# Kernel optimization log

Hardware: AMD Instinct MI355X
Metric: run time of the kernel (lower is better)

Reference implementation:

```python
import jax, jax.numpy as jnp
import numpy as np

NEG_INF = -jnp.inf


def setup_inputs() -> dict:
    key = jax.random.key(0)
    k1, k2, k3 = jax.random.split(key, 3)
    b, d, n_classes = 8192, 512, 100
    x = jax.random.normal(k1, (b, d), dtype=jnp.float32)
    y = jax.random.randint(k2, (b,), 0, n_classes, dtype=jnp.int64)
    T = jax.random.uniform(k3, (), dtype=jnp.float32)
    return {"x": x, "y": y, "T": T}


def reference(x, y, T):
    b = x.shape[0]
    # normalize by (unbiased, like torch) std of the whole tensor
    xs = x / jnp.std(x, ddof=1)
    # pairwise euclidean distance via gram matrix: ||xi-xj||^2 = ni + nj - 2 xi.xj
    sqn = jnp.sum(xs * xs, axis=1)                      # [b]
    sqd = sqn[:, None] + sqn[None, :] - 2.0 * (xs @ xs.T)  # [b, b]
    sqd = jnp.maximum(sqd, 0.0)
    eye = jnp.eye(b, dtype=bool)
    # diagonal is masked out later; replace 0 with 1 before sqrt for safe grads
    dist = jnp.sqrt(jnp.where(eye, 1.0, sqd))           # [b, b]
    e_dist = -dist * jnp.power(10.0, T)                 # [b, b]
    # denominator: all pairs except self
    den_dist = jnp.where(eye, NEG_INF, e_dist)
    # numerator: same-label pairs except self (inv=False)
    same = (y[:, None] == y[None, :]) & (~eye)
    num_dist = jnp.where(same, e_dist, NEG_INF)
    num = jax.nn.logsumexp(num_dist, axis=1)            # [b]
    den = jax.nn.logsumexp(den_dist, axis=1)            # [b]
    # rows with no positives (num = -inf) are zeroed out, as in the torch code
    bad = jnp.isinf(num)
    num = jnp.where(bad, 0.0, num)
    den = jnp.where(bad, 0.0, den)
    return -jnp.mean(num - den)
```

## Files before the change

### kernel.cpp

```cpp
#include <hip/hip_runtime.h>


#define NROW 8192
#define NDIM 512
#define BM   128
#define BK   32
#define NKT  (NDIM / BK)
#define NT   (NROW / BM)
#define NBLK (NT * (NT + 1) / 2)
#define TILE (BM * BK)

typedef __attribute__((ext_vector_type(8))) short bf16x8;
typedef __attribute__((ext_vector_type(4))) float f32x4;

#define NEG_INF (-__builtin_inff())

static const size_t WS_SCAL = 4096;
static const size_t WS_XB   = 8192;
static const size_t WS_SQN  = WS_XB + (size_t)NROW * NDIM * 2;
static const size_t WS_RS   = WS_SQN + (size_t)NROW * 4;
static const size_t WS_P4   = WS_RS + (size_t)NROW * 4;

__device__ __forceinline__ unsigned short f2bf(float f) {
    unsigned int u = __float_as_uint(f);
    u += 0x7FFFu + ((u >> 16) & 1u);
    return (unsigned short)(u >> 16);
}

#define GLD_LDS16(gp, lp) __builtin_amdgcn_global_load_lds( \
    (const __attribute__((address_space(1))) unsigned int*)(gp), \
    (__attribute__((address_space(3))) unsigned int*)(lp), 16, 0, 0)

__global__ __launch_bounds__(256) void k_norm(const float* __restrict__ x,
                                              unsigned short* __restrict__ xb,
                                              float* __restrict__ sqn,
                                              float* __restrict__ rsum) {
    int w = threadIdx.x >> 6, lane = threadIdx.x & 63;
    int row = blockIdx.x * 4 + w;
    const float4* xr = (const float4*)(x + (size_t)row * NDIM);
    ushort4* xo = (ushort4*)(xb + (size_t)row * NDIM);
    float ss = 0.f, s1 = 0.f;
#pragma unroll
    for (int ph = 0; ph < 2; ++ph) {
        float4 v = xr[ph * 64 + lane];
        ss += v.x * v.x + v.y * v.y + v.z * v.z + v.w * v.w;
        s1 += (v.x + v.y) + (v.z + v.w);
        xo[ph * 64 + lane] = make_ushort4(f2bf(v.x), f2bf(v.y), f2bf(v.z), f2bf(v.w));
    }
#pragma unroll
    for (int off = 32; off >= 1; off >>= 1) {
        ss += __shfl_xor(ss, off, 64);
        s1 += __shfl_xor(s1, off, 64);
    }
    if (lane == 0) { sqn[row] = ss; rsum[row] = s1; }
}

__global__ __launch_bounds__(256) void k_prep(const float* __restrict__ sqn,
                                              const float* __restrict__ rsum,
                                              float* __restrict__ scal,
                                              float* __restrict__ out) {
    int t = threadIdx.x;
    double s = 0.0, ss = 0.0;
    for (int i = t; i < NROW; i += 256) { s += (double)rsum[i]; ss += (double)sqn[i]; }
#pragma unroll
    for (int off = 32; off >= 1; off >>= 1) {
        s  += __shfl_xor(s, off, 64);
        ss += __shfl_xor(ss, off, 64);
    }
    __shared__ double sa[4], sb[4];
    int w = t >> 6, lane = t & 63;
    if (lane == 0) { sa[w] = s; sb[w] = ss; }
    __syncthreads();
    if (t == 0) {
        double S = sa[0] + sa[1] + sa[2] + sa[3];
        double SS = sb[0] + sb[1] + sb[2] + sb[3];
        const double N = (double)NROW * (double)NDIM;
        double var = (SS - S * S / N) / (N - 1.0);
        scal[0] = (float)(1.0 / sqrt(var));
        out[0] = 0.f;
    }
}

__global__ __launch_bounds__(256, 3) void k_main(const unsigned short* __restrict__ xb,
                                                 const float* __restrict__ sqn,
                                                 const int* __restrict__ y,
                                                 const float* __restrict__ Tp,
                                                 const float* __restrict__ scal,
                                                 float4* __restrict__ part) {
    __shared__ __attribute__((aligned(16))) unsigned short lds[3][2][TILE];
    float4* P    = (float4*)&lds[0][0][0];
    float4* redC = P + 2048;

    int bid = blockIdx.x;
    int L = (bid & 7) * (NBLK / 8) + (bid >> 3);
    int RT = 0;
    for (;;) { int cnt = 36 + 64 * (7 - RT); if (L < cnt) break; L -= cnt; ++RT; }
    int rt, ct;
    if (L < 36) {
        int i = 0;
        while (L >= 8 - i) { L -= 8 - i; ++i; }
        rt = RT * 8 + i; ct = RT * 8 + i + L;
    } else {
        L -= 36;
        int CT = RT + 1 + (L >> 6), cc = L & 63;
        rt = RT * 8 + (cc >> 3); ct = CT * 8 + (cc & 7);
    }
    const bool diag = (rt == ct);

    const int tid = threadIdx.x;
    const int w = tid >> 6, lane = tid & 63;
    const int wr = w >> 1, wc = w & 1;
    const int g = lane >> 4, qq = lane & 15;
    const int rowTile = rt * BM, colTile = ct * BM;

    const int q0 = w * 2, q1 = w * 2 + 1;
    const int colg = ((lane & 3) ^ ((lane >> 3) & 3)) * 8;
    const int sr = lane >> 2;
    const unsigned short* gA0 = xb + (size_t)(rowTile + q0 * 16 + sr) * NDIM + colg;
    const unsigned short* gA1 = xb + (size_t)(rowTile + q1 * 16 + sr) * NDIM + colg;
    const unsigned short* gB0 = xb + (size_t)(colTile + q0 * 16 + sr) * NDIM + colg;
    const unsigned short* gB1 = xb + (size_t)(colTile + q1 * 16 + sr) * NDIM + colg;

#define STAGE_T(buf, ke) do { \
    GLD_LDS16(gA0 + (ke), &lds[buf][0][q0 * 512]); \
    GLD_LDS16(gA1 + (ke), &lds[buf][0][q1 * 512]); \
    GLD_LDS16(gB0 + (ke), &lds[buf][1][q0 * 512]); \
    GLD_LDS16(gB1 + (ke), &lds[buf][1][q1 * 512]); } while (0)

    const int kx = (g ^ ((qq >> 1) & 3)) * 8;
    const int aoff = (wr * 64 + qq) * BK + kx;
    const int boff = (wc * 64 + qq) * BK + kx;

    f32x4 acc[4][4];
    const f32x4 zero = {0.f, 0.f, 0.f, 0.f};
#pragma unroll
    for (int i = 0; i < 4; ++i)
#pragma unroll
        for (int j = 0; j < 4; ++j) acc[i][j] = zero;

    STAGE_T(0, 0);
    STAGE_T(1, BK);

    int c = 0;
    for (int kt = 0; kt < NKT; ++kt) {
        if (kt + 2 < NKT) {
            int sb = c + 2; if (sb >= 3) sb -= 3;
            STAGE_T(sb, (kt + 2) * BK);
            asm volatile("s_waitcnt vmcnt(8)" ::: "memory");
        } else if (kt + 1 < NKT) {
            asm volatile("s_waitcnt vmcnt(4)" ::: "memory");
        } else {
            asm volatile("s_waitcnt vmcnt(0)" ::: "memory");
        }
        __builtin_amdgcn_s_barrier();

        const unsigned short* AA = &lds[c][0][0];
        const unsigned short* BB = &lds[c][1][0];
        bf16x8 af[4], bfr[4];
#pragma unroll
        for (int mi = 0; mi < 4; ++mi)
            af[mi] = *(const bf16x8*)&AA[aoff + mi * 16 * BK];
#pragma unroll
        for (int ni = 0; ni < 4; ++ni)
            bfr[ni] = *(const bf16x8*)&BB[boff + ni * 16 * BK];
        __builtin_amdgcn_s_setprio(1);
#pragma unroll
        for (int mi = 0; mi < 4; ++mi)
#pragma unroll
            for (int ni = 0; ni < 4; ++ni)
                acc[mi][ni] = __builtin_amdgcn_mfma_f32_16x16x32_bf16(
                    af[mi], bfr[ni], acc[mi][ni], 0, 0, 0);
        __builtin_amdgcn_s_setprio(0);
        asm volatile("s_waitcnt lgkmcnt(0)" ::: "memory");
        __builtin_amdgcn_s_barrier();
        c += 1; if (c == 3) c = 0;
    }

    const float c2 = scal[0] * __builtin_amdgcn_exp2f(Tp[0] * 3.321928094887362f)
                             * 1.4426950408889634f;
    float scol[4]; int ycol[4];
#pragma unroll
    for (int ni = 0; ni < 4; ++ni) {
        int C = colTile + wc * 64 + ni * 16 + qq;
        scol[ni] = sqn[C];
        ycol[ni] = y[C];
    }

    unsigned mm0 = 0, mm1 = 0;
#pragma unroll
    for (int mi = 0; mi < 4; ++mi) {
        float srow4[4]; int yrow4[4];
#pragma unroll
        for (int r = 0; r < 4; ++r) {
            int R = rowTile + wr * 64 + mi * 16 + g * 4 + r;
            srow4[r] = sqn[R];
            yrow4[r] = y[R];
        }
#pragma unroll
        for (int r = 0; r < 4; ++r) {
            const int R = rowTile + wr * 64 + mi * 16 + g * 4 + r;
#pragma unroll
            for (int ni = 0; ni < 4; ++ni) {
                const int C = colTile + wc * 64 + ni * 16 + qq;
                float sq = fmaf(-2.f, acc[mi][ni][r], srow4[r] + scol[ni]);
                sq = fmaxf(sq, 0.f);
                float s2 = -__builtin_amdgcn_sqrtf(sq) * c2;
                if (R == C) s2 = NEG_INF;
                acc[mi][ni][r] = s2;
                unsigned bit = (yrow4[r] == ycol[ni]) ? 1u : 0u;
                int idx = ((mi & 1) * 4 + r) * 4 + ni;
                if (mi < 2) mm0 |= bit << idx; else mm1 |= bit << idx;
            }
        }
    }

    if (wr == 0) {
#pragma unroll
        for (int mi = 0; mi < 4; ++mi) {
            unsigned mmw = (mi < 2) ? mm0 : mm1;
#pragma unroll
            for (int r = 0; r < 4; ++r) {
                float m_l = fmaxf(fmaxf(acc[mi][0][r], acc[mi][1][r]),
                                  fmaxf(acc[mi][2][r], acc[mi][3][r]));
                float ld = 0.f, ln = 0.f;
#pragma unroll
                for (int ni = 0; ni < 4; ++ni) {
                    float e = __builtin_amdgcn_exp2f(acc[mi][ni][r] - m_l);
                    ld += e;
                    ln += ((mmw >> (((mi & 1) * 4 + r) * 4 + ni)) & 1) ? e : 0.f;
                }
                int lr = mi * 16 + g * 4 + r;
                P[(wc * 16 + qq) * 64 + (lr ^ qq)] = make_float4(m_l, ld, ln, 0.f);
            }
        }
    }
    __syncthreads();
    if (w == 0) {
        float M = NEG_INF, Ls = 0.f, Ln = 0.f;
#pragma unroll
        for (int wcx = 0; wcx < 2; ++wcx)
#pragma unroll
            for (int q = 0; q < 16; ++q) {
                float4 p = P[(wcx * 16 + q) * 64 + (lane ^ q)];
                if (p.x > M) {
                    float s = __builtin_amdgcn_exp2f(M - p.x);
                    Ls *= s; Ln *= s; M = p.x;
                }
                float e = __builtin_amdgcn_exp2f(p.x - M);
                Ls += p.y * e; Ln += p.z * e;
            }
        part[(size_t)ct * NROW + rowTile + lane] = make_float4(M, Ls, Ln, 0.f);
    }
    __syncthreads();
    if (wr == 1) {
#pragma unroll
        for (int mi = 0; mi < 4; ++mi) {
            unsigned mmw = (mi < 2) ? mm0 : mm1;
#pragma unroll
            for (int r = 0; r < 4; ++r) {
                float m_l = fmaxf(fmaxf(acc[mi][0][r], acc[mi][1][r]),
                                  fmaxf(acc[mi][2][r], acc[mi][3][r]));
                float ld = 0.f, ln = 0.f;
#pragma unroll
                for (int ni = 0; ni < 4; ++ni) {
                    float e = __builtin_amdgcn_exp2f(acc[mi][ni][r] - m_l);
                    ld += e;
                    ln += ((mmw >> (((mi & 1) * 4 + r) * 4 + ni)) & 1) ? e : 0.f;
                }
                int lr = mi * 16 + g * 4 + r;
                P[(wc * 16 + qq) * 64 + (lr ^ qq)] = make_float4(m_l, ld, ln, 0.f);
            }
        }
    }
    __syncthreads();
    if (w == 2) {
        float M = NEG_INF, Ls = 0.f, Ln = 0.f;
#pragma unroll
        for (int wcx = 0; wcx < 2; ++wcx)
#pragma unroll
            for (int q = 0; q < 16; ++q) {
                float4 p = P[(wcx * 16 + q) * 64 + (lane ^ q)];
                if (p.x > M) {
                    float s = __builtin_amdgcn_exp2f(M - p.x);
                    Ls *= s; Ln *= s; M = p.x;
                }
                float e = __builtin_amdgcn_exp2f(p.x - M);
                Ls += p.y * e; Ln += p.z * e;
            }
        part[(size_t)ct * NROW + rowTile + 64 + lane] = make_float4(M, Ls, Ln, 0.f);
    }

    if (!diag) {
        __syncthreads();
#pragma unroll
        for (int ni = 0; ni < 4; ++ni) {
            float mx = NEG_INF;
#pragma unroll
            for (int mi = 0; mi < 4; ++mi)
#pragma unroll
                for (int r = 0; r < 4; ++r) mx = fmaxf(mx, acc[mi][ni][r]);
            mx = fmaxf(mx, __shfl_xor(mx, 16, 64));
            mx = fmaxf(mx, __shfl_xor(mx, 32, 64));
            float ld = 0.f, ln = 0.f;
#pragma unroll
            for (int mi = 0; mi < 4; ++mi) {
                unsigned mmw = (mi < 2) ? mm0 : mm1;
#pragma unroll
                for (int r = 0; r < 4; ++r) {
                    float e = __builtin_amdgcn_exp2f(acc[mi][ni][r] - mx);
                    ld += e;
                    ln += ((mmw >> (((mi & 1) * 4 + r) * 4 + ni)) & 1) ? e : 0.f;
                }
            }
            ld += __shfl_xor(ld, 16, 64); ld += __shfl_xor(ld, 32, 64);
            ln += __shfl_xor(ln, 16, 64); ln += __shfl_xor(ln, 32, 64);
            if (g == 0) {
                int lc = wc * 64 + ni * 16 + qq;
                redC[lc * 2 + wr] = make_float4(mx, ld, ln, 0.f);
            }
        }
        __syncthreads();
        if (tid < BM) {
            float4 a = redC[tid * 2 + 0], b = redC[tid * 2 + 1];
            float M = fmaxf(a.x, b.x);
            float e0 = __builtin_amdgcn_exp2f(a.x - M), e1 = __builtin_amdgcn_exp2f(b.x - M);
            part[(size_t)rt * NROW + colTile + tid] =
                make_float4(M, a.y * e0 + b.y * e1, a.z * e0 + b.z * e1, 0.f);
        }
    }
#undef STAGE_T
}

__global__ __launch_bounds__(256) void k_rows(const float4* __restrict__ part,
                                              float* __restrict__ out) {
    int r = blockIdx.x * 256 + threadIdx.x;
    float M = NEG_INF, Ls = 0.f, Ln = 0.f;
    for (int ctt = 0; ctt < NT; ++ctt) {
        float4 p = part[(size_t)ctt * NROW + r];
        if (p.x > M) {
            float sc = __builtin_amdgcn_exp2f(M - p.x);
            Ls *= sc; Ln *= sc; M = p.x;
        }
        float s2 = __builtin_amdgcn_exp2f(p.x - M);
        Ls += p.y * s2;
        Ln += p.z * s2;
    }
    float v = (Ln > 0.f) ? (__builtin_amdgcn_logf(Ln) - __builtin_amdgcn_logf(Ls))
                               * 0.69314718055994530942f
                         : 0.f;
#pragma unroll
    for (int off = 32; off >= 1; off >>= 1) v += __shfl_xor(v, off, 64);
    __shared__ float sa[4];
    int w = threadIdx.x >> 6, lane = threadIdx.x & 63;
    if (lane == 0) sa[w] = v;
    __syncthreads();
    if (threadIdx.x == 0)
        atomicAdd(out, -((sa[0] + sa[1] + sa[2] + sa[3]) / (float)NROW));
}

extern "C" void kernel_launch(void* const* d_in, const int* in_sizes, int n_in,
                              void* d_out, int out_size, void* d_ws, size_t ws_size,
                              hipStream_t stream) {
    (void)in_sizes; (void)n_in; (void)out_size; (void)ws_size;
    const float* x  = (const float*)d_in[0];
    const int*   y  = (const int*)d_in[1];
    const float* Tp = (const float*)d_in[2];
    float* out = (float*)d_out;

    char* ws = (char*)d_ws;
    float*          scal = (float*)(ws + WS_SCAL);
    unsigned short* xb   = (unsigned short*)(ws + WS_XB);
    float*          sqn  = (float*)(ws + WS_SQN);
    float*          rsum = (float*)(ws + WS_RS);
    float4*         p4   = (float4*)(ws + WS_P4);

    k_norm <<<NROW / 4, 256, 0, stream>>>(x, xb, sqn, rsum);
    k_prep <<<1, 256, 0, stream>>>(sqn, rsum, scal, out);
    k_main <<<NBLK, 256, 0, stream>>>(xb, sqn, y, Tp, scal, p4);
    k_rows <<<NROW / 256, 256, 0, stream>>>(p4, out);
}
```

Before: 99.96 us.

## Use a single tile-wide max for logsumexp partials and share exps

Rather than computing separate per-row and per-column maxima and exponentials, the epilogue now reduces one maximum over the whole 128x128 tile and exponentiates each score once. Those exponentials feed both the row and column partial sums. This removes the duplicated exp pass for the transposed (column) contribution, drops several barriers by merging the two half-tile reduction phases, and shrinks the LDS records to float2. The trade-off is numerical: entries far below the tile maximum can underflow to zero where a per-row maximum would have kept them, and a row whose only positives are tiny could then lose them.

Result: faster. 82.93 us, median of 2 (-17.0%).

```diff
diff --git a/kernel.cpp b/kernel.cpp
--- a/kernel.cpp
+++ b/kernel.cpp
@@ -88,8 +88,9 @@
                                                  const float* __restrict__ scal,
                                                  float4* __restrict__ part) {
     __shared__ __attribute__((aligned(16))) unsigned short lds[3][2][TILE];
-    float4* P    = (float4*)&lds[0][0][0];
-    float4* redC = P + 2048;
+    float2* P    = (float2*)&lds[0][0][0];
+    float2* redC = (float2*)((char*)&lds[0][0][0] + 32768);
+    float*  mxw  = (float*)((char*)&lds[0][0][0] + 34816);
 
     int bid = blockIdx.x;
     int L = (bid & 7) * (NBLK / 8) + (bid >> 3);
@@ -187,6 +188,7 @@
     }
 
     unsigned mm0 = 0, mm1 = 0;
+    float tmax = NEG_INF;
 #pragma unroll
     for (int mi = 0; mi < 4; ++mi) {
         float srow4[4]; int yrow4[4];
@@ -207,126 +209,74 @@
                 float s2 = -__builtin_amdgcn_sqrtf(sq) * c2;
                 if (R == C) s2 = NEG_INF;
                 acc[mi][ni][r] = s2;
+                tmax = fmaxf(tmax, s2);
                 unsigned bit = (yrow4[r] == ycol[ni]) ? 1u : 0u;
                 int idx = ((mi & 1) * 4 + r) * 4 + ni;
                 if (mi < 2) mm0 |= bit << idx; else mm1 |= bit << idx;
             }
         }
     }
-
-    if (wr == 0) {
-#pragma unroll
-        for (int mi = 0; mi < 4; ++mi) {
-            unsigned mmw = (mi < 2) ? mm0 : mm1;
-#pragma unroll
-            for (int r = 0; r < 4; ++r) {
-                float m_l = fmaxf(fmaxf(acc[mi][0][r], acc[mi][1][r]),
-                                  fmaxf(acc[mi][2][r], acc[mi][3][r]));
-                float ld = 0.f, ln = 0.f;
-#pragma unroll
-                for (int ni = 0; ni < 4; ++ni) {
-                    float e = __builtin_amdgcn_exp2f(acc[mi][ni][r] - m_l);
-                    ld += e;
-                    ln += ((mmw >> (((mi & 1) * 4 + r) * 4 + ni)) & 1) ? e : 0.f;
-                }
-                int lr = mi * 16 + g * 4 + r;
-                P[(wc * 16 + qq) * 64 + (lr ^ qq)] = make_float4(m_l, ld, ln, 0.f);
+#pragma unroll
+    for (int off = 1; off <= 32; off <<= 1) tmax = fmaxf(tmax, __shfl_xor(tmax, off, 64));
+    if (lane == 0) mxw[w] = tmax;
+    __syncthreads();
+    const float Mt = fmaxf(fmaxf(mxw[0], mxw[1]), fmaxf(mxw[2], mxw[3]));
+
+#pragma unroll
+    for (int mi = 0; mi < 4; ++mi) {
+        unsigned mmw = (mi < 2) ? mm0 : mm1;
+#pragma unroll
+        for (int r = 0; r < 4; ++r) {
+            float ld = 0.f, ln = 0.f;
+#pragma unroll
+            for (int ni = 0; ni < 4; ++ni) {
+                float e = __builtin_amdgcn_exp2f(acc[mi][ni][r] - Mt);
+                acc[mi][ni][r] = e;
+                ld += e;
+                ln += ((mmw >> (((mi & 1) * 4 + r) * 4 + ni)) & 1) ? e : 0.f;
             }
-        }
-    }
-    __syncthreads();
-    if (w == 0) {
-        float M = NEG_INF, Ls = 0.f, Ln = 0.f;
-#pragma unroll
-        for (int wcx = 0; wcx < 2; ++wcx)
-#pragma unroll
-            for (int q = 0; q < 16; ++q) {
-                float4 p = P[(wcx * 16 + q) * 64 + (lane ^ q)];
-                if (p.x > M) {
-                    float s = __builtin_amdgcn_exp2f(M - p.x);
-                    Ls *= s; Ln *= s; M = p.x;
-                }
-                float e = __builtin_amdgcn_exp2f(p.x - M);
-                Ls += p.y * e; Ln += p.z * e;
-            }
-        part[(size_t)ct * NROW + rowTile + lane] = make_float4(M, Ls, Ln, 0.f);
-    }
-    __syncthreads();
-    if (wr == 1) {
-#pragma unroll
-        for (int mi = 0; mi < 4; ++mi) {
-            unsigned mmw = (mi < 2) ? mm0 : mm1;
-#pragma unroll
-            for (int r = 0; r < 4; ++r) {
-                float m_l = fmaxf(fmaxf(acc[mi][0][r], acc[mi][1][r]),
-                                  fmaxf(acc[mi][2][r], acc[mi][3][r]));
-                float ld = 0.f, ln = 0.f;
-#pragma unroll
-                for (int ni = 0; ni < 4; ++ni) {
-                    float e = __builtin_amdgcn_exp2f(acc[mi][ni][r] - m_l);
-                    ld += e;
-                    ln += ((mmw >> (((mi & 1) * 4 + r) * 4 + ni)) & 1) ? e : 0.f;
-                }
-                int lr = mi * 16 + g * 4 + r;
-                P[(wc * 16 + qq) * 64 + (lr ^ qq)] = make_float4(m_l, ld, ln, 0.f);
-            }
-        }
-    }
-    __syncthreads();
-    if (w == 2) {
-        float M = NEG_INF, Ls = 0.f, Ln = 0.f;
-#pragma unroll
-        for (int wcx = 0; wcx < 2; ++wcx)
-#pragma unroll
-            for (int q = 0; q < 16; ++q) {
-                float4 p = P[(wcx * 16 + q) * 64 + (lane ^ q)];
-                if (p.x > M) {
-                    float s = __builtin_amdgcn_exp2f(M - p.x);
-                    Ls *= s; Ln *= s; M = p.x;
-                }
-                float e = __builtin_amdgcn_exp2f(p.x - M);
-                Ls += p.y * e; Ln += p.z * e;
-            }
-        part[(size_t)ct * NROW + rowTile + 64 + lane] = make_float4(M, Ls, Ln, 0.f);
-    }
-
+            int lr = mi * 16 + g * 4 + r;
+            P[((wr * 2 + wc) * 16 + qq) * 64 + (lr ^ qq)] = make_float2(ld, ln);
+        }
+    }
     if (!diag) {
-        __syncthreads();
 #pragma unroll
         for (int ni = 0; ni < 4; ++ni) {
-            float mx = NEG_INF;
-#pragma unroll
-            for (int mi = 0; mi < 4; ++mi)
-#pragma unroll
-                for (int r = 0; r < 4; ++r) mx = fmaxf(mx, acc[mi][ni][r]);
-            mx = fmaxf(mx, __shfl_xor(mx, 16, 64));
-            mx = fmaxf(mx, __shfl_xor(mx, 32, 64));
-            float ld = 0.f, ln = 0.f;
+            float sd = 0.f, sn = 0.f;
 #pragma unroll
             for (int mi = 0; mi < 4; ++mi) {
                 unsigned mmw = (mi < 2) ? mm0 : mm1;
 #pragma unroll
                 for (int r = 0; r < 4; ++r) {
-                    float e = __builtin_amdgcn_exp2f(acc[mi][ni][r] - mx);
-                    ld += e;
-                    ln += ((mmw >> (((mi & 1) * 4 + r) * 4 + ni)) & 1) ? e : 0.f;
+                    float e = acc[mi][ni][r];
+                    sd += e;
+                    sn += ((mmw >> (((mi & 1) * 4 + r) * 4 + ni)) & 1) ? e : 0.f;
                 }
             }
-            ld += __shfl_xor(ld, 16, 64); ld += __shfl_xor(ld, 32, 64);
-            ln += __shfl_xor(ln, 16, 64); ln += __shfl_xor(ln, 32, 64);
-            if (g == 0) {
-                int lc = wc * 64 + ni * 16 + qq;
-                redC[lc * 2 + wr] = make_float4(mx, ld, ln, 0.f);
+            sd += __shfl_xor(sd, 16, 64); sd += __shfl_xor(sd, 32, 64);
+            sn += __shfl_xor(sn, 16, 64); sn += __shfl_xor(sn, 32, 64);
+            if (g == 0) redC[(wc * 64 + ni * 16 + qq) * 2 + wr] = make_float2(sd, sn);
+        }
+    }
+    __syncthreads();
+
+    if (w == 0 || w == 2) {
+        const int wrh = w >> 1;
+        float Ls = 0.f, Ln = 0.f;
+#pragma unroll
+        for (int wcx = 0; wcx < 2; ++wcx)
+#pragma unroll
+            for (int q = 0; q < 16; ++q) {
+                float2 p = P[((wrh * 2 + wcx) * 16 + q) * 64 + (lane ^ q)];
+                Ls += p.x; Ln += p.y;
             }
-        }
-        __syncthreads();
-        if (tid < BM) {
-            float4 a = redC[tid * 2 + 0], b = redC[tid * 2 + 1];
-            float M = fmaxf(a.x, b.x);
-            float e0 = __builtin_amdgcn_exp2f(a.x - M), e1 = __builtin_amdgcn_exp2f(b.x - M);
-            part[(size_t)rt * NROW + colTile + tid] =
-                make_float4(M, a.y * e0 + b.y * e1, a.z * e0 + b.z * e1, 0.f);
-        }
+        part[(size_t)ct * NROW + rowTile + wrh * 64 + lane] =
+            make_float4(Mt, Ls, Ln, 0.f);
+    }
+    if (!diag && tid < BM) {
+        float2 a = redC[tid * 2 + 0], b = redC[tid * 2 + 1];
+        part[(size_t)rt * NROW + colTile + tid] =
+            make_float4(Mt, a.x + b.x, a.y + b.y, 0.f);
     }
 #undef STAGE_T
 }
```
